# Performance work log

Hardware: AMD Instinct MI355X
Metric: run time of the kernel (lower is better)

Reference implementation:

```python
import jax, jax.numpy as jnp
import numpy as np

N = 50000   # nodes
D = 64      # feature_dim
E = 800000  # edges per edge set
NEG_SLOPE = 0.2  # PyG GATConv default


def gat_conv(x, edge_index, W, a_src, a_dst, bias):
    """PyG GATConv, heads=1, concat=True, add_self_loops=True.
    h = x W; e_{j->i} = leakyrelu(a_src.h_j + a_dst.h_i); segment-softmax over dst.
    """
    n = x.shape[0]
    h = x @ W                                   # [N, D]
    s = h @ a_src                               # [N] per-node src score
    d = h @ a_dst                               # [N] per-node dst score
    src, dst = edge_index[0], edge_index[1]
    e = jax.nn.leaky_relu(s[src] + d[dst], NEG_SLOPE)
    # remove_self_loops: mask any pre-existing self loops out of the softmax
    e = jnp.where(src == dst, jnp.float32(-1e9), e)
    # add_self_loops: one (i, i) edge per node
    loop = jnp.arange(n)
    src_all = jnp.concatenate([src, loop])
    dst_all = jnp.concatenate([dst, loop])
    e_all = jnp.concatenate([e, jax.nn.leaky_relu(s + d, NEG_SLOPE)])
    # numerically stable segment softmax over incoming edges of each dst node
    m = jax.ops.segment_max(e_all, dst_all, num_segments=n)
    p = jnp.exp(e_all - m[dst_all])
    denom = jax.ops.segment_sum(p, dst_all, num_segments=n)
    alpha = p / denom[dst_all]                  # [E + N]
    out = jax.ops.segment_sum(alpha[:, None] * h[src_all], dst_all, num_segments=n)
    return out + bias


def encode(x, edge_a, edge_b, W, a_src, a_dst, bias):
    # Original overwrites x_a/x_b each loop iteration, always reading the
    # original x, so only the final-layer encoder's single application survives.
    x_a = jax.nn.relu(gat_conv(x, edge_a, W, a_src, a_dst, bias))
    x_b = jax.nn.relu(gat_conv(x, edge_b, W, a_src, a_dst, bias))
    return x_a, x_b


def setup_inputs() -> dict:
    key = jax.random.key(0)
    ks = jax.random.split(key, 13)
    edges = [jax.random.randint(ks[i], (2, E), 0, N) for i in range(8)]
    x = jax.random.normal(ks[8], (N, D), dtype=jnp.float32)
    scale = np.float32(1.0 / np.sqrt(D))
    W = jax.random.normal(ks[9], (4, D, D), dtype=jnp.float32) * scale
    a_src = jax.random.normal(ks[10], (4, D), dtype=jnp.float32) * scale
    a_dst = jax.random.normal(ks[11], (4, D), dtype=jnp.float32) * scale
    bias = jnp.zeros((4, D), dtype=jnp.float32)
    return {"edge_tp_a": edges[0], "edge_tp_b": edges[1], "edge_tn_a": edges[2],
            "edge_tn_b": edges[3], "edge_dp_a": edges[4], "edge_dp_b": edges[5],
            "edge_dn_a": edges[6], "edge_dn_b": edges[7], "x": x, "W": W,
            "a_src": a_src, "a_dst": a_dst, "bias": bias}


def reference(edge_tp_a, edge_tp_b, edge_tn_a, edge_tn_b, edge_dp_a, edge_dp_b,
              edge_dn_a, edge_dn_b, x, W, a_src, a_dst, bias):
    # 4 encode calls, each with its own (fresh) GATConv parameters
    tp_a, tp_b = encode(x, edge_tp_a, edge_tp_b, W[0], a_src[0], a_dst[0], bias[0])
    tn_a, tn_b = encode(x, edge_tn_a, edge_tn_b, W[1], a_src[1], a_dst[1], bias[1])
    dp_a, dp_b = encode(x, edge_dp_a, edge_dp_b, W[2], a_src[2], a_dst[2], bias[2])
    dn_a, dn_b = encode(x, edge_dn_a, edge_dn_b, W[3], a_src[3], a_dst[3], bias[3])
    # original return order
    return (tp_a, tp_b, dp_a, dp_b, tn_a, tn_b, dn_a, dn_b)
```

## Files before the change

### kernel.cpp

```cpp
#include <hip/hip_runtime.h>
#include <hip/hip_bf16.h>

typedef unsigned int u32;
typedef unsigned short u16;
typedef __hip_bfloat16 bf16;

typedef __attribute__((ext_vector_type(8))) short short8;
typedef __attribute__((ext_vector_type(4))) float float4v;

#define CAP 5120

__device__ __forceinline__ float lrelu(float v) { return v > 0.f ? v : 0.2f * v; }

__device__ __forceinline__ u16 f2b(float f) {
  u32 x = __float_as_uint(f);
  u32 r = (x + 0x7fffu + ((x >> 16) & 1u)) >> 16;
  return (u16)r;
}
__device__ __forceinline__ float b2fbits(u16 b) {
  return __uint_as_float(((u32)b) << 16);
}
__device__ __forceinline__ float blo(u32 v) { return __uint_as_float(v << 16); }
__device__ __forceinline__ float bhi(u32 v) { return __uint_as_float(v & 0xffff0000u); }

struct EdgePtrs { const int* e[8]; };

__global__ __launch_bounds__(256) void CSGDN_32031866093637_kernel(u32* __restrict__ p,
                                                                   int count) {
  int i = blockIdx.x * 256 + threadIdx.x;
  if (i < count) p[i] = 0;
}

__global__ __launch_bounds__(256) void gemm_kernel(
    const float* __restrict__ x, const float* __restrict__ W,
    const float* __restrict__ a_src, const float* __restrict__ a_dst,
    u16* __restrict__ H, float* __restrict__ sv, float* __restrict__ dv, int n) {
  const int p = blockIdx.y;
  const int tid = threadIdx.x, lane = tid & 63, wv = tid >> 6;
  const int rowbase = blockIdx.x * 64;
  __shared__ short xl[64 * 72];
  __shared__ short wl[64 * 72];
#pragma unroll
  for (int it = 0; it < 16; it++) {
    int idx = it * 256 + tid;
    int r = idx >> 6, c = idx & 63;
    int gr = rowbase + r; if (gr > n - 1) gr = n - 1;
    xl[r * 72 + c] = (short)f2b(x[(size_t)gr * 64 + c]);
  }
#pragma unroll
  for (int it = 0; it < 16; it++) {
    int idx = it * 256 + tid;
    int k = idx >> 6, nc = idx & 63;
    wl[nc * 72 + k] = (short)f2b(W[p * 4096 + k * 64 + nc]);
  }
  __syncthreads();

  const int q = lane >> 4, c15 = lane & 15;
  const int wrow0 = wv * 16;
  short8 af0 = *(const short8*)&xl[(wrow0 + c15) * 72 + 0 * 32 + q * 8];
  short8 af1 = *(const short8*)&xl[(wrow0 + c15) * 72 + 1 * 32 + q * 8];
  float4v acc[4];
#pragma unroll
  for (int nt = 0; nt < 4; nt++) {
    acc[nt] = (float4v){0.f, 0.f, 0.f, 0.f};
    short8 b0 = *(const short8*)&wl[(nt * 16 + c15) * 72 + 0 * 32 + q * 8];
    short8 b1 = *(const short8*)&wl[(nt * 16 + c15) * 72 + 1 * 32 + q * 8];
    acc[nt] = __builtin_amdgcn_mfma_f32_16x16x32_bf16(af0, b0, acc[nt], 0, 0, 0);
    acc[nt] = __builtin_amdgcn_mfma_f32_16x16x32_bf16(af1, b1, acc[nt], 0, 0, 0);
  }
  u16* Hb = H + (size_t)p * n * 64;
  float as4[4], ad4[4];
#pragma unroll
  for (int nt = 0; nt < 4; nt++) {
    as4[nt] = a_src[p * 64 + nt * 16 + c15];
    ad4[nt] = a_dst[p * 64 + nt * 16 + c15];
  }
#pragma unroll
  for (int r = 0; r < 4; r++) {
    int row_g = rowbase + wrow0 + q * 4 + r;
    bool ok = row_g < n;
#pragma unroll
    for (int nt = 0; nt < 4; nt++) {
      if (ok) Hb[(size_t)row_g * 64 + nt * 16 + c15] = f2b(acc[nt][r]);
    }
    float ps = 0.f, pd = 0.f;
#pragma unroll
    for (int nt = 0; nt < 4; nt++) {
      ps = fmaf(acc[nt][r], as4[nt], ps);
      pd = fmaf(acc[nt][r], ad4[nt], pd);
    }
#pragma unroll
    for (int o = 1; o < 16; o <<= 1) {
      ps += __shfl_xor(ps, o, 64);
      pd += __shfl_xor(pd, o, 64);
    }
    if (ok && c15 == 0) {
      sv[(size_t)p * n + row_g] = ps;
      dv[(size_t)p * n + row_g] = pd;
    }
  }
}

__global__ __launch_bounds__(256) void bin_kernel(EdgePtrs ep, u32* __restrict__ gcnt,
                                                  u32* __restrict__ bbuf, int E, int nb) {
  int set = blockIdx.y;
  const int* e = ep.e[set];
  __shared__ u32 hist[256], gbase[256], loffs[257], curs[256];
  __shared__ u32 sorted[4096];
  int tid = threadIdx.x, lane = tid & 63, wv = tid >> 6;
  hist[tid] = 0;
  curs[tid] = 0;
  __syncthreads();
  int start = blockIdx.x * 4096;
  u32 pk_r[16];
#pragma unroll
  for (int t = 0; t < 16; t++) {
    int i = start + t * 256 + tid;
    u32 pk = 0xffffffffu;
    if (i < E) {
      int s = e[i], d = e[E + i];
      if (s != d) {
        pk = ((u32)d << 16) | (u32)s;
        atomicAdd(&hist[d >> 8], 1u);
      }
    }
    pk_r[t] = pk;
  }
  __syncthreads();
  if (hist[tid] > 0) gbase[tid] = atomicAdd(&gcnt[set * nb + tid], hist[tid]);
  if (wv == 0) {
    u32 carry = 0;
    for (int base = 0; base < 256; base += 64) {
      u32 v = hist[base + lane], x = v;
#pragma unroll
      for (int o = 1; o < 64; o <<= 1) { u32 y = __shfl_up(x, o, 64); if (lane >= o) x += y; }
      loffs[base + lane] = carry + x - v;
      carry += __shfl(x, 63, 64);
    }
    if (lane == 0) loffs[256] = carry;
  }
  __syncthreads();
#pragma unroll
  for (int t = 0; t < 16; t++) {
    u32 pk = pk_r[t];
    if (pk != 0xffffffffu) {
      int b = pk >> 24;
      u32 pos = loffs[b] + atomicAdd(&curs[b], 1u);
      sorted[pos] = pk;
    }
  }
  __syncthreads();
  int cnt = (int)loffs[256];
  for (int j = tid; j < cnt; j += 256) {
    u32 pk = sorted[j];
    int b = pk >> 24;
    u32 gpos = gbase[b] + ((u32)j - loffs[b]);
    if (gpos >= CAP) gpos = CAP - 1;
    bbuf[((size_t)(set * nb + b)) * CAP + gpos] = pk;
  }
}

__global__ __launch_bounds__(512) void agg_kernel(
    const u32* __restrict__ gcnt, const u32* __restrict__ bbuf,
    const u16* __restrict__ H, const float* __restrict__ sv,
    const float* __restrict__ dv, const float* __restrict__ bias,
    float* __restrict__ out, int n, int nb) {
  const int omap[8] = {0, 1, 4, 5, 2, 3, 6, 7};
  int b = blockIdx.x, set = blockIdx.y, p = set >> 1;
  int tid = threadIdx.x, lane = tid & 63, wv = tid >> 6;
  int node0 = b << 8;
  int nn = min(256, n - node0);
  __shared__ u16 ss[CAP];
  __shared__ float spe[CAP];
  __shared__ u32 hist[256], offs[257], curs[256];
  __shared__ float dpw[256], spw[256];
  const float* sp = sv + (size_t)p * n;
  const float* dp = dv + (size_t)p * n;
  for (int i = tid; i < 256; i += 512) { hist[i] = 0; curs[i] = 0; }
  for (int i = tid; i < nn; i += 512) { dpw[i] = dp[node0 + i]; spw[i] = sp[node0 + i]; }
  __syncthreads();
  int cnt = (int)gcnt[set * nb + b];
  if (cnt > CAP) cnt = CAP;
  const u32* eb = bbuf + ((size_t)(set * nb + b)) * CAP;
  u32 pk_r[10];
  float pe_r[10];
#pragma unroll
  for (int t = 0; t < 10; t++) {
    int j = t * 512 + tid;
    u32 pk = 0;
    float pe = 0.f;
    if (j < cnt) {
      pk = eb[j];
      int s = pk & 0xffff, dl = (pk >> 16) & 255;
      atomicAdd(&hist[dl], 1u);
      pe = __expf(lrelu(sp[s] + dpw[dl]));
    }
    pk_r[t] = pk;
    pe_r[t] = pe;
  }
  __syncthreads();
  if (wv == 0) {
    u32 carry = 0;
    for (int base = 0; base < 256; base += 64) {
      u32 v = hist[base + lane];
      u32 x = v;
#pragma unroll
      for (int o = 1; o < 64; o <<= 1) { u32 y = __shfl_up(x, o, 64); if (lane >= o) x += y; }
      offs[base + lane] = carry + x - v;
      carry += __shfl(x, 63, 64);
    }
    if (lane == 0) offs[256] = carry;
  }
  __syncthreads();
#pragma unroll
  for (int t = 0; t < 10; t++) {
    int j = t * 512 + tid;
    if (j < cnt) {
      u32 pk = pk_r[t];
      int dl = (pk >> 16) & 255;
      u32 pos = offs[dl] + atomicAdd(&curs[dl], 1u);
      ss[pos] = (u16)(pk & 0xffff);
      spe[pos] = pe_r[t];
    }
  }
  __syncthreads();
  const u16* Hp = H + (size_t)p * n * 64;
  const int g = lane >> 3, sub = lane & 7;
  float4v bv0 = *(const float4v*)&bias[p * 64 + sub * 8];
  float4v bv1 = *(const float4v*)&bias[p * 64 + sub * 8 + 4];
  float* op = out + (size_t)omap[set] * n * 64;
  for (int r0 = 0; r0 < nn; r0 += 64) {
    int i = r0 + wv * 8 + g;
    bool valid = i < nn;
    int iv = valid ? i : 0;
    int beg = (int)offs[iv], end2 = (int)offs[iv + 1];
    int cntg = valid ? (end2 - beg) : 0;
    int node = node0 + iv;
    float pself = valid ? __expf(lrelu(spw[iv] + dpw[iv])) : 0.f;
    uint4 hs = *(const uint4*)(Hp + ((size_t)node << 6) + (sub << 3));
    float den = pself;
    float a0 = pself * blo(hs.x), a1 = pself * bhi(hs.x);
    float a2 = pself * blo(hs.y), a3 = pself * bhi(hs.y);
    float a4 = pself * blo(hs.z), a5 = pself * bhi(hs.z);
    float a6 = pself * blo(hs.w), a7 = pself * bhi(hs.w);
    int tmax = cntg;
#pragma unroll
    for (int o = 8; o < 64; o <<= 1) tmax = max(tmax, __shfl_xor(tmax, o, 64));
    for (int t = 0; t < tmax; t += 2) {
      bool act0 = t < cntg, act1 = t + 1 < cntg;
      int j0 = act0 ? beg + t : 0;
      int j1 = act1 ? beg + t + 1 : 0;
      float pe0 = act0 ? spe[j0] : 0.f;
      float pe1 = act1 ? spe[j1] : 0.f;
      int s0 = ss[j0], s1 = ss[j1];
      uint4 hv0 = *(const uint4*)(Hp + ((size_t)s0 << 6) + (sub << 3));
      uint4 hv1 = *(const uint4*)(Hp + ((size_t)s1 << 6) + (sub << 3));
      a0 = fmaf(pe0, blo(hv0.x), a0); a1 = fmaf(pe0, bhi(hv0.x), a1);
      a2 = fmaf(pe0, blo(hv0.y), a2); a3 = fmaf(pe0, bhi(hv0.y), a3);
      a4 = fmaf(pe0, blo(hv0.z), a4); a5 = fmaf(pe0, bhi(hv0.z), a5);
      a6 = fmaf(pe0, blo(hv0.w), a6); a7 = fmaf(pe0, bhi(hv0.w), a7);
      den += pe0;
      a0 = fmaf(pe1, blo(hv1.x), a0); a1 = fmaf(pe1, bhi(hv1.x), a1);
      a2 = fmaf(pe1, blo(hv1.y), a2); a3 = fmaf(pe1, bhi(hv1.y), a3);
      a4 = fmaf(pe1, blo(hv1.z), a4); a5 = fmaf(pe1, bhi(hv1.z), a5);
      a6 = fmaf(pe1, blo(hv1.w), a6); a7 = fmaf(pe1, bhi(hv1.w), a7);
      den += pe1;
    }
    if (valid) {
      float rd = 1.f / den;
      float4v o0 = {fmaxf(fmaf(a0, rd, bv0.x), 0.f), fmaxf(fmaf(a1, rd, bv0.y), 0.f),
                    fmaxf(fmaf(a2, rd, bv0.z), 0.f), fmaxf(fmaf(a3, rd, bv0.w), 0.f)};
      float4v o1 = {fmaxf(fmaf(a4, rd, bv1.x), 0.f), fmaxf(fmaf(a5, rd, bv1.y), 0.f),
                    fmaxf(fmaf(a6, rd, bv1.z), 0.f), fmaxf(fmaf(a7, rd, bv1.w), 0.f)};
      *(float4v*)&op[((size_t)node << 6) + (sub << 3)] = o0;
      *(float4v*)&op[((size_t)node << 6) + (sub << 3) + 4] = o1;
    }
  }
}

extern "C" void kernel_launch(void* const* d_in, const int* in_sizes, int n_in,
                              void* d_out, int out_size, void* d_ws, size_t ws_size,
                              hipStream_t stream) {
  const int E = in_sizes[0] / 2;
  const int n = in_sizes[8] / 64;
  const int nb = (n + 255) >> 8;
  const float* x = (const float*)d_in[8];
  const float* W = (const float*)d_in[9];
  const float* a_src = (const float*)d_in[10];
  const float* a_dst = (const float*)d_in[11];
  const float* bias = (const float*)d_in[12];
  float* out = (float*)d_out;

  char* ws = (char*)d_ws;
  auto alloc = [&](size_t bytes) {
    char* p = ws;
    ws += (bytes + 255) & ~(size_t)255;
    return p;
  };
  u16* H = (u16*)alloc((size_t)4 * n * 64 * 2);
  float* sv = (float*)alloc((size_t)4 * n * 4);
  float* dv = (float*)alloc((size_t)4 * n * 4);
  u32* gcnt = (u32*)alloc((size_t)8 * nb * 4);
  u32* bbuf = (u32*)alloc((size_t)8 * nb * CAP * 4);

  EdgePtrs ep;
  for (int i = 0; i < 8; i++) ep.e[i] = (const int*)d_in[i];

  dim3 b256(256);
  CSGDN_32031866093637_kernel<<<(8 * nb + 255) / 256, b256, 0, stream>>>(gcnt, 8 * nb);
  gemm_kernel<<<dim3((n + 63) / 64, 4), b256, 0, stream>>>(x, W, a_src, a_dst, H, sv, dv, n);
  bin_kernel<<<dim3((E + 4095) / 4096, 8), b256, 0, stream>>>(ep, gcnt, bbuf, E, nb);
  agg_kernel<<<dim3(nb, 8), dim3(512), 0, stream>>>(gcnt, bbuf, H, sv, dv, bias, out, n, nb);
}
```

Measured before the change: 343.0 us.

## Merge GEMM and edge-binning into one role-split kernel, unroll gather by four

The projection GEMM and the edge-binning pass now run as two roles inside a single launch that shares one shared-memory buffer, with the block index choosing the role. This removes a kernel boundary and lets the two independent stages overlap on the GPU. The aggregation grid is flattened so the eight edge sets for one node bucket sit next to each other in launch order, and its gather loop is unrolled from two to four edges per step to keep more independent H loads in flight. The costs are extra registers in the aggregation loop, which may lower occupancy, and more wasted lanes when edge counts are not a multiple of four.

```diff
diff --git a/kernel.cpp b/kernel.cpp
--- a/kernel.cpp
+++ b/kernel.cpp
@@ -31,15 +31,16 @@
   if (i < count) p[i] = 0;
 }
 
-__global__ __launch_bounds__(256) void gemm_kernel(
-    const float* __restrict__ x, const float* __restrict__ W,
+
+__device__ __forceinline__ void gemm_role(
+    u32* smem, int g, const float* __restrict__ x, const float* __restrict__ W,
     const float* __restrict__ a_src, const float* __restrict__ a_dst,
     u16* __restrict__ H, float* __restrict__ sv, float* __restrict__ dv, int n) {
-  const int p = blockIdx.y;
+  const int p = g & 3;
+  const int rowbase = (g >> 2) * 64;
   const int tid = threadIdx.x, lane = tid & 63, wv = tid >> 6;
-  const int rowbase = blockIdx.x * 64;
-  __shared__ short xl[64 * 72];
-  __shared__ short wl[64 * 72];
+  short* xl = (short*)smem;
+  short* wl = xl + 64 * 72;
 #pragma unroll
   for (int it = 0; it < 16; it++) {
     int idx = it * 256 + tid;
@@ -101,17 +102,21 @@
   }
 }
 
-__global__ __launch_bounds__(256) void bin_kernel(EdgePtrs ep, u32* __restrict__ gcnt,
-                                                  u32* __restrict__ bbuf, int E, int nb) {
-  int set = blockIdx.y;
+__device__ __forceinline__ void bin_role(
+    u32* smem, int bf, EdgePtrs ep, u32* __restrict__ gcnt, u32* __restrict__ bbuf,
+    int E, int nb) {
+  int set = bf & 7, chunk = bf >> 3;
   const int* e = ep.e[set];
-  __shared__ u32 hist[256], gbase[256], loffs[257], curs[256];
-  __shared__ u32 sorted[4096];
+  u32* hist = smem;
+  u32* gbase = smem + 256;
+  u32* curs = smem + 512;
+  u32* loffs = smem + 768;
+  u32* sorted = smem + 1028;
   int tid = threadIdx.x, lane = tid & 63, wv = tid >> 6;
   hist[tid] = 0;
   curs[tid] = 0;
   __syncthreads();
-  int start = blockIdx.x * 4096;
+  int start = chunk * 4096;
   u32 pk_r[16];
 #pragma unroll
   for (int t = 0; t < 16; t++) {
@@ -160,13 +165,26 @@
   }
 }
 
+__global__ __launch_bounds__(256) void prep_kernel(
+    EdgePtrs ep, u32* __restrict__ gcnt, u32* __restrict__ bbuf, int E, int nb,
+    int nbin,
+    const float* __restrict__ x, const float* __restrict__ W,
+    const float* __restrict__ a_src, const float* __restrict__ a_dst,
+    u16* __restrict__ H, float* __restrict__ sv, float* __restrict__ dv, int n) {
+  __shared__ __align__(16) u32 smem[5248];
+  int f = blockIdx.x;
+  if (f < nbin) bin_role(smem, f, ep, gcnt, bbuf, E, nb);
+  else gemm_role(smem, f - nbin, x, W, a_src, a_dst, H, sv, dv, n);
+}
+
 __global__ __launch_bounds__(512) void agg_kernel(
     const u32* __restrict__ gcnt, const u32* __restrict__ bbuf,
     const u16* __restrict__ H, const float* __restrict__ sv,
     const float* __restrict__ dv, const float* __restrict__ bias,
     float* __restrict__ out, int n, int nb) {
   const int omap[8] = {0, 1, 4, 5, 2, 3, 6, 7};
-  int b = blockIdx.x, set = blockIdx.y, p = set >> 1;
+  int f = blockIdx.x;
+  int set = f & 7, b = f >> 3, p = set >> 1;
   int tid = threadIdx.x, lane = tid & 63, wv = tid >> 6;
   int node0 = b << 8;
   int nn = min(256, n - node0);
@@ -246,25 +264,38 @@
     int tmax = cntg;
 #pragma unroll
     for (int o = 8; o < 64; o <<= 1) tmax = max(tmax, __shfl_xor(tmax, o, 64));
-    for (int t = 0; t < tmax; t += 2) {
-      bool act0 = t < cntg, act1 = t + 1 < cntg;
-      int j0 = act0 ? beg + t : 0;
-      int j1 = act1 ? beg + t + 1 : 0;
-      float pe0 = act0 ? spe[j0] : 0.f;
-      float pe1 = act1 ? spe[j1] : 0.f;
-      int s0 = ss[j0], s1 = ss[j1];
+    for (int t = 0; t < tmax; t += 4) {
+      bool c0 = t < cntg, c1 = t + 1 < cntg, c2 = t + 2 < cntg, c3 = t + 3 < cntg;
+      int j0 = c0 ? beg + t : 0;
+      int j1 = c1 ? beg + t + 1 : 0;
+      int j2 = c2 ? beg + t + 2 : 0;
+      int j3 = c3 ? beg + t + 3 : 0;
+      float pe0 = c0 ? spe[j0] : 0.f;
+      float pe1 = c1 ? spe[j1] : 0.f;
+      float pe2 = c2 ? spe[j2] : 0.f;
+      float pe3 = c3 ? spe[j3] : 0.f;
+      int s0 = ss[j0], s1 = ss[j1], s2 = ss[j2], s3 = ss[j3];
       uint4 hv0 = *(const uint4*)(Hp + ((size_t)s0 << 6) + (sub << 3));
       uint4 hv1 = *(const uint4*)(Hp + ((size_t)s1 << 6) + (sub << 3));
+      uint4 hv2 = *(const uint4*)(Hp + ((size_t)s2 << 6) + (sub << 3));
+      uint4 hv3 = *(const uint4*)(Hp + ((size_t)s3 << 6) + (sub << 3));
       a0 = fmaf(pe0, blo(hv0.x), a0); a1 = fmaf(pe0, bhi(hv0.x), a1);
       a2 = fmaf(pe0, blo(hv0.y), a2); a3 = fmaf(pe0, bhi(hv0.y), a3);
       a4 = fmaf(pe0, blo(hv0.z), a4); a5 = fmaf(pe0, bhi(hv0.z), a5);
       a6 = fmaf(pe0, blo(hv0.w), a6); a7 = fmaf(pe0, bhi(hv0.w), a7);
-      den += pe0;
       a0 = fmaf(pe1, blo(hv1.x), a0); a1 = fmaf(pe1, bhi(hv1.x), a1);
       a2 = fmaf(pe1, blo(hv1.y), a2); a3 = fmaf(pe1, bhi(hv1.y), a3);
       a4 = fmaf(pe1, blo(hv1.z), a4); a5 = fmaf(pe1, bhi(hv1.z), a5);
       a6 = fmaf(pe1, blo(hv1.w), a6); a7 = fmaf(pe1, bhi(hv1.w), a7);
-      den += pe1;
+      a0 = fmaf(pe2, blo(hv2.x), a0); a1 = fmaf(pe2, bhi(hv2.x), a1);
+      a2 = fmaf(pe2, blo(hv2.y), a2); a3 = fmaf(pe2, bhi(hv2.y), a3);
+      a4 = fmaf(pe2, blo(hv2.z), a4); a5 = fmaf(pe2, bhi(hv2.z), a5);
+      a6 = fmaf(pe2, blo(hv2.w), a6); a7 = fmaf(pe2, bhi(hv2.w), a7);
+      a0 = fmaf(pe3, blo(hv3.x), a0); a1 = fmaf(pe3, bhi(hv3.x), a1);
+      a2 = fmaf(pe3, blo(hv3.y), a2); a3 = fmaf(pe3, bhi(hv3.y), a3);
+      a4 = fmaf(pe3, blo(hv3.z), a4); a5 = fmaf(pe3, bhi(hv3.z), a5);
+      a6 = fmaf(pe3, blo(hv3.w), a6); a7 = fmaf(pe3, bhi(hv3.w), a7);
+      den += (pe0 + pe1) + (pe2 + pe3);
     }
     if (valid) {
       float rd = 1.f / den;
@@ -306,9 +337,13 @@
   EdgePtrs ep;
   for (int i = 0; i < 8; i++) ep.e[i] = (const int*)d_in[i];
 
+  const int ebpb = (E + 4095) / 4096;
+  const int nbin = 8 * ebpb;
+  const int ngemm = ((n + 63) / 64) * 4;
+
   dim3 b256(256);
   CSGDN_32031866093637_kernel<<<(8 * nb + 255) / 256, b256, 0, stream>>>(gcnt, 8 * nb);
-  gemm_kernel<<<dim3((n + 63) / 64, 4), b256, 0, stream>>>(x, W, a_src, a_dst, H, sv, dv, n);
-  bin_kernel<<<dim3((E + 4095) / 4096, 8), b256, 0, stream>>>(ep, gcnt, bbuf, E, nb);
-  agg_kernel<<<dim3(nb, 8), dim3(512), 0, stream>>>(gcnt, bbuf, H, sv, dv, bias, out, n, nb);
-}
+  prep_kernel<<<nbin + ngemm, b256, 0, stream>>>(ep, gcnt, bbuf, E, nb, nbin,
+                                                 x, W, a_src, a_dst, H, sv, dv, n);
+  agg_kernel<<<nb * 8, dim3(512), 0, stream>>>(gcnt, bbuf, H, sv, dv, bias, out, n, nb);
+}
```

Result: faster. 294.8 us (-14.1%).
